# Optimization experiments

Measured on AMD Instinct MI355X. Metric: run time of the kernel, lower is better.

Reference implementation:

```python
import jax, jax.numpy as jnp
import numpy as np

D = 1024
H = 16
DH = D // H


def setup_inputs() -> dict:
    key = jax.random.key(0)
    ks = jax.random.split(key, 7)
    s = 0.02
    return {
        "z": jax.random.normal(ks[0], (8, 1024, D), dtype=jnp.float32),
        "ln_w": jnp.ones((D,), dtype=jnp.float32),
        "ln_b": jnp.zeros((D,), dtype=jnp.float32),
        "W_qkv": jax.random.normal(ks[1], (D, 3 * D), dtype=jnp.float32) * s,
        "b_qkv": jnp.zeros((3 * D,), dtype=jnp.float32),
        "W_proj": jax.random.normal(ks[2], (D, D), dtype=jnp.float32) * s,
        "b_proj": jnp.zeros((D,), dtype=jnp.float32),
    }


def reference(z, ln_w, ln_b, W_qkv, b_qkv, W_proj, b_proj):
    b, n, d = z.shape
    # Pre-LN
    mu = jnp.mean(z, axis=-1, keepdims=True)
    var = jnp.var(z, axis=-1, keepdims=True)
    zn = (z - mu) / jnp.sqrt(var + 1e-5) * ln_w + ln_b
    # QKV projection: [b, n, 3, H, DH]
    qkv = (zn @ W_qkv + b_qkv).reshape(b, n, 3, H, DH)
    q = qkv[:, :, 0].transpose(0, 2, 1, 3)  # [b, H, n, DH]
    k = qkv[:, :, 1].transpose(0, 2, 1, 3)
    v = qkv[:, :, 2].transpose(0, 2, 1, 3)
    scale = 1.0 / jnp.sqrt(jnp.asarray(DH, dtype=z.dtype))
    scores = jnp.einsum("bhqd,bhkd->bhqk", q, k) * scale
    attn = jax.nn.softmax(scores, axis=-1)
    msa = jnp.einsum("bhqk,bhkd->bhqd", attn, v)  # [b, H, n, DH]
    msa_cat = msa.transpose(0, 2, 1, 3).reshape(b, n, d)
    out = msa_cat @ W_proj + b_proj
    return z + out
```

## Files before the change

### kernel.cpp

```cpp
#include <hip/hip_runtime.h>
#include <stdint.h>

typedef unsigned short u16;
typedef uint8_t u8;
typedef __bf16 bf16x8 __attribute__((ext_vector_type(8)));
typedef float f32x4 __attribute__((ext_vector_type(4)));
typedef int i32x8 __attribute__((ext_vector_type(8)));

#define D_MODEL 1024
#define NHEADS  16
#define DHEAD   64
#define BATCH   8
#define SEQ     1024
#define MTOT    (BATCH*SEQ)

#define GPTR(p) ((const __attribute__((address_space(1))) void*)(p))
#define LPTR(p) ((__attribute__((address_space(3))) void*)(p))

#if defined(__HIP_DEVICE_COMPILE__)
  #define MFMA_FP8_16x16x128(a, b, c) \
      __builtin_amdgcn_mfma_scale_f32_16x16x128_f8f6f4((a), (b), (c), 0, 0, 0, 127, 0, 127)
  #define CVT_PK_FP8(a, b, old, w) __builtin_amdgcn_cvt_pk_fp8_f32((a), (b), (old), (w))
#else
  #define MFMA_FP8_16x16x128(a, b, c) (c)
  #define CVT_PK_FP8(a, b, old, w) (0)
#endif

__device__ __forceinline__ u16 f2bf(float f) {
    union { float f; uint32_t u; } v; v.f = f;
    uint32_t u = v.u;
    u += 0x7fffu + ((u >> 16) & 1u);
    return (u16)(u >> 16);
}

__device__ __forceinline__ uint32_t pklo(int i1, int i0) {
    return __builtin_amdgcn_perm((uint32_t)i1, (uint32_t)i0, 0x05040100u);
}

__global__ __launch_bounds__(256) void prep_inputs(
    const float* __restrict__ z, const float* __restrict__ w,
    const float* __restrict__ b, uint32_t* __restrict__ znf,
    const float* __restrict__ Wqkv, const float* __restrict__ Wproj,
    u8* __restrict__ outQkv, u8* __restrict__ outProj)
{
    __shared__ float red[8];
    __shared__ u8 tile[32][36];
    const int bid = blockIdx.x;
    const int t = threadIdx.x;
    if (bid < MTOT) {
        const int row = bid;
        const float4 v = reinterpret_cast<const float4*>(z + (size_t)row * D_MODEL)[t];
        float s  = v.x + v.y + v.z + v.w;
        float s2 = v.x*v.x + v.y*v.y + v.z*v.z + v.w*v.w;
        #pragma unroll
        for (int off = 32; off; off >>= 1) {
            s  += __shfl_down(s,  off, 64);
            s2 += __shfl_down(s2, off, 64);
        }
        const int wave = t >> 6, lane = t & 63;
        if (lane == 0) { red[wave] = s; red[wave + 4] = s2; }
        __syncthreads();
        if (t == 0) {
            float ts  = red[0] + red[1] + red[2] + red[3];
            float ts2 = red[4] + red[5] + red[6] + red[7];
            float mu  = ts * (1.0f / D_MODEL);
            float var = ts2 * (1.0f / D_MODEL) - mu * mu;
            red[0] = mu; red[1] = rsqrtf(var + 1e-5f);
        }
        __syncthreads();
        const float mu = red[0], rstd = red[1];
        const float4 wv = reinterpret_cast<const float4*>(w)[t];
        const float4 bv = reinterpret_cast<const float4*>(b)[t];
        const float x0 = (v.x - mu) * rstd * wv.x + bv.x;
        const float x1 = (v.y - mu) * rstd * wv.y + bv.y;
        const float x2 = (v.z - mu) * rstd * wv.z + bv.z;
        const float x3 = (v.w - mu) * rstd * wv.w + bv.w;
        int pk = CVT_PK_FP8(x0, x1, 0, false);
        pk = CVT_PK_FP8(x2, x3, pk, true);
        znf[(size_t)row * (D_MODEL / 4) + t] = (uint32_t)pk;
    } else {
        const int bx = bid - MTOT;
        const int cx = bx & 127;
        const int r0 = (bx >> 7) * 32;
        const float* in; u8* out; int C;
        if (cx < 96) { in = Wqkv;  out = outQkv;  C = 3072; }
        else         { in = Wproj; out = outProj; C = 1024; }
        const int c0 = (cx < 96 ? cx : cx - 96) * 32;
        const int tx = t & 31, ty = t >> 5;
        #pragma unroll
        for (int i = 0; i < 4; ++i) {
            const float f = in[(size_t)(r0 + ty + i*8) * C + c0 + tx];
            tile[ty + i*8][tx] = (u8)(CVT_PK_FP8(f, 0.f, 0, false) & 0xFF);
        }
        __syncthreads();
        #pragma unroll
        for (int i = 0; i < 4; ++i)
            out[(size_t)(c0 + ty + i*8) * D_MODEL + r0 + tx] = tile[tx][ty + i*8];
    }
}

#define QSCALE 23.0831207f

#define GEMM_PRELUDE                                                            \
    const int tid = threadIdx.x;                                                \
    const int wave = tid >> 6, lane = tid & 63;                                 \
    const int lm = lane & 15, g = lane >> 4;                                    \
    const int wm = (wave >> 1) * 64, wn = (wave & 1) * 64;                      \
    const int m0 = blockIdx.y * 128;                                            \
    const int srow = tid >> 3;                                                  \
    const int sseg = tid & 7;                                                   \
    const int sgcol = (sseg ^ (srow & 7)) * 16;                                 \
    const int xl = lm & 7;                                                      \
    const int ca0 = ((2 * g) ^ xl) * 16;                                        \
    const int ca1 = ((2 * g + 1) ^ xl) * 16;

#define FP8_KLOOP(As_, Bs_, A_, Bt_, n0_, MFMA_STMT)                            \
    f32x4 acc[4][4] = {};                                                       \
    for (int k0 = 0; k0 < D_MODEL; k0 += 128) {                                 \
        _Pragma("unroll")                                                       \
        for (int c = 0; c < 4; ++c) {                                           \
            const int r = srow + c * 32;                                        \
            __builtin_amdgcn_global_load_lds(                                   \
                GPTR(&A_[(size_t)(m0 + r) * D_MODEL + k0 + sgcol]),             \
                LPTR(&As_[r * 128 + sseg * 16]), 16, 0, 0);                     \
            __builtin_amdgcn_global_load_lds(                                   \
                GPTR(&Bt_[(size_t)((n0_) + r) * D_MODEL + k0 + sgcol]),         \
                LPTR(&Bs_[r * 128 + sseg * 16]), 16, 0, 0);                     \
        }                                                                       \
        __syncthreads();                                                        \
        i32x8 af[4], bfr[4];                                                    \
        _Pragma("unroll")                                                       \
        for (int i = 0; i < 4; ++i) {                                           \
            const uint4 alo = *reinterpret_cast<const uint4*>(&As_[(wm + i*16 + lm) * 128 + ca0]); \
            const uint4 ahi = *reinterpret_cast<const uint4*>(&As_[(wm + i*16 + lm) * 128 + ca1]); \
            af[i][0] = alo.x; af[i][1] = alo.y; af[i][2] = alo.z; af[i][3] = alo.w; \
            af[i][4] = ahi.x; af[i][5] = ahi.y; af[i][6] = ahi.z; af[i][7] = ahi.w; \
            const uint4 blo = *reinterpret_cast<const uint4*>(&Bs_[(wn + i*16 + lm) * 128 + ca0]); \
            const uint4 bhi = *reinterpret_cast<const uint4*>(&Bs_[(wn + i*16 + lm) * 128 + ca1]); \
            bfr[i][0] = blo.x; bfr[i][1] = blo.y; bfr[i][2] = blo.z; bfr[i][3] = blo.w; \
            bfr[i][4] = bhi.x; bfr[i][5] = bhi.y; bfr[i][6] = bhi.z; bfr[i][7] = bhi.w; \
        }                                                                       \
        _Pragma("unroll")                                                       \
        for (int i = 0; i < 4; ++i)                                             \
            _Pragma("unroll")                                                   \
            for (int j = 0; j < 4; ++j)                                         \
                MFMA_STMT;                                                      \
        __syncthreads();                                                        \
    }

__global__ __launch_bounds__(256, 2) void gemm_qkv(
    const u8* __restrict__ A, const u8* __restrict__ Bt,
    const float* __restrict__ bias,
    u16* __restrict__ q, u16* __restrict__ k, u16* __restrict__ vT)
{
    __shared__ u8 As[128 * 128];
    __shared__ u8 Bs[128 * 128];
    GEMM_PRELUDE
    const int bx = blockIdx.x;
    if (bx < 16) {
        const int n0 = bx * 128;
        FP8_KLOOP(As, Bs, A, Bt, n0, acc[i][j] = MFMA_FP8_16x16x128(bfr[j], af[i], acc[i][j]))
        const int colbase = n0 + wn;
        const int sel = colbase >> 10;
        const int h = (colbase & 1023) >> 6;
        u16* dst = (sel == 0) ? q : k;
        const float scl = (sel == 0) ? QSCALE : 1.0f;
        #pragma unroll
        for (int j = 0; j < 4; ++j) {
            const int dh0 = j * 16 + 4 * g;
            const float4 bv4 = *reinterpret_cast<const float4*>(&bias[colbase + dh0]);
            #pragma unroll
            for (int i = 0; i < 4; ++i) {
                const int m = m0 + wm + i * 16 + lm;
                const int b = m >> 10, t = m & 1023;
                ushort4 o;
                o.x = f2bf((acc[i][j][0] + bv4.x) * scl);
                o.y = f2bf((acc[i][j][1] + bv4.y) * scl);
                o.z = f2bf((acc[i][j][2] + bv4.z) * scl);
                o.w = f2bf((acc[i][j][3] + bv4.w) * scl);
                *reinterpret_cast<ushort4*>(
                    &dst[(((size_t)(b * NHEADS + h)) * SEQ + t) * DHEAD + dh0]) = o;
            }
        }
    } else {
        const int n0 = 2048 + (bx - 16) * 128;
        FP8_KLOOP(As, Bs, A, Bt, n0, acc[i][j] = MFMA_FP8_16x16x128(af[i], bfr[j], acc[i][j]))
        const int vcol = (n0 - 2048) + wn;
        const int h = vcol >> 6;
        #pragma unroll
        for (int j = 0; j < 4; ++j) {
            const int dh = ((vcol & 63) + j * 16) + lm;
            const float bv = bias[2048 + vcol + j * 16 + lm];
            #pragma unroll
            for (int i = 0; i < 4; ++i) {
                const int t0 = m0 + wm + i * 16 + 4 * g;
                const int b = t0 >> 10, t = t0 & 1023;
                ushort4 o;
                o.x = f2bf(acc[i][j][0] + bv);
                o.y = f2bf(acc[i][j][1] + bv);
                o.z = f2bf(acc[i][j][2] + bv);
                o.w = f2bf(acc[i][j][3] + bv);
                *reinterpret_cast<ushort4*>(
                    &vT[(((size_t)(b * NHEADS + h)) * DHEAD + dh) * SEQ + t]) = o;
            }
        }
    }
}

__global__ __launch_bounds__(256, 2) void gemm_proj(
    const u8* __restrict__ A, const u8* __restrict__ Bt,
    const float* __restrict__ bias, const float* __restrict__ z,
    float* __restrict__ out)
{
    __shared__ u8 As[128 * 128];
    __shared__ u8 Bs[128 * 128];
    GEMM_PRELUDE
    const int n0 = blockIdx.x * 128;
    FP8_KLOOP(As, Bs, A, Bt, n0, acc[i][j] = MFMA_FP8_16x16x128(bfr[j], af[i], acc[i][j]))
    #pragma unroll
    for (int j = 0; j < 4; ++j) {
        const int col0 = n0 + wn + j * 16 + 4 * g;
        const float4 bv4 = *reinterpret_cast<const float4*>(&bias[col0]);
        #pragma unroll
        for (int i = 0; i < 4; ++i) {
            const int m = m0 + wm + i * 16 + lm;
            const size_t idx = (size_t)m * D_MODEL + col0;
            const float4 zv = *reinterpret_cast<const float4*>(&z[idx]);
            float4 ov;
            ov.x = zv.x + acc[i][j][0] + bv4.x;
            ov.y = zv.y + acc[i][j][1] + bv4.y;
            ov.z = zv.z + acc[i][j][2] + bv4.z;
            ov.w = zv.w + acc[i][j][3] + bv4.w;
            *reinterpret_cast<float4*>(&out[idx]) = ov;
        }
    }
}

#define KLD 68
#define EXP2_MAGIC 12582912.0f

__global__ __launch_bounds__(256, 4) void attn_kernel(
    const u16* __restrict__ Q, const u16* __restrict__ K,
    const u16* __restrict__ Vt, u8* __restrict__ msaf)
{
    __shared__ u16 Ks[2][64 * KLD];
    __shared__ u16 Vs[2][64 * KLD];
    const int tid = threadIdx.x, wave = tid >> 6, lane = tid & 63;
    const int lm = lane & 15, g = lane >> 4;
    const int bi = blockIdx.x;
    const int bh = bi & 127;
    const int q0 = (bi >> 7) * 128;
    const int b = bh >> 4, h = bh & 15;
    const size_t headBase = (size_t)bh * SEQ * DHEAD;
    const u16* Qh = Q + headBase;
    const u16* Kh = K + headBase;
    const u16* Vh = Vt + headBase;

    const int srow = tid >> 3, sseg = tid & 7;
    const int aA = 16 * (sseg >> 2) + 4 * (sseg & 3);

    const uint4 onesu = {0x3F803F80u, 0x3F803F80u, 0x3F803F80u, 0x3F803F80u};
    const bf16x8 ONES = __builtin_bit_cast(bf16x8, onesu);
    const f32x4 SMINIT = {16250.0f, 16250.0f, 16250.0f, 16250.0f};

    bf16x8 qf[2][2];
    #pragma unroll
    for (int s = 0; s < 2; ++s) {
        const u16* qrow = Qh + (size_t)(q0 + s * 64 + wave * 16 + lm) * DHEAD;
        qf[s][0] = *reinterpret_cast<const bf16x8*>(qrow + g * 8);
        qf[s][1] = *reinterpret_cast<const bf16x8*>(qrow + 32 + g * 8);
    }

    f32x4 o[2][4] = {};
    f32x4 lacc[2] = {};

    for (int j0 = 0; j0 < SEQ; j0 += 128) {
        #pragma unroll
        for (int hb = 0; hb < 2; ++hb) {
            const int jj = j0 + hb * 64;
            #pragma unroll
            for (int s2 = 0; s2 < 2; ++s2) {
                const int row = srow + 32 * s2;
                *reinterpret_cast<uint4*>(&Ks[hb][row * KLD + sseg * 8]) =
                    *reinterpret_cast<const uint4*>(&Kh[(size_t)(jj + row) * DHEAD + sseg * 8]);
                const u16* vrow = Vh + (size_t)row * SEQ + jj;
                const uint2 va = *reinterpret_cast<const uint2*>(vrow + aA);
                const uint2 vb = *reinterpret_cast<const uint2*>(vrow + 32 + aA);
                uint4 wv; wv.x = va.x; wv.y = va.y; wv.z = vb.x; wv.w = vb.y;
                *reinterpret_cast<uint4*>(&Vs[hb][row * KLD + sseg * 8]) = wv;
            }
        }
        __syncthreads();

        #pragma unroll
        for (int hb = 0; hb < 2; ++hb) {
            bf16x8 kf0[4], kf1[4];
            #pragma unroll
            for (int ni = 0; ni < 4; ++ni) {
                kf0[ni] = *reinterpret_cast<const bf16x8*>(&Ks[hb][(ni*16 + lm) * KLD + g * 8]);
                kf1[ni] = *reinterpret_cast<const bf16x8*>(&Ks[hb][(ni*16 + lm) * KLD + 32 + g * 8]);
            }

            bf16x8 pfr[2][2];
            #pragma unroll
            for (int s = 0; s < 2; ++s) {
                f32x4 st[4];
                __builtin_amdgcn_s_setprio(1);
                #pragma unroll
                for (int ni = 0; ni < 4; ++ni) {
                    st[ni] = __builtin_amdgcn_mfma_f32_16x16x32_bf16(kf0[ni], qf[s][0], SMINIT, 0, 0, 0);
                    st[ni] = __builtin_amdgcn_mfma_f32_16x16x32_bf16(kf1[ni], qf[s][1], st[ni], 0, 0, 0);
                }
                __builtin_amdgcn_s_setprio(0);
                int ip[4][4];
                #pragma unroll
                for (int ni = 0; ni < 4; ++ni)
                    #pragma unroll
                    for (int r = 0; r < 4; ++r)
                        ip[ni][r] = __builtin_bit_cast(int, st[ni][r] + EXP2_MAGIC);
                #pragma unroll
                for (int c = 0; c < 2; ++c) {
                    uint4 u;
                    u.x = pklo(ip[c][1],   ip[c][0]);
                    u.y = pklo(ip[c][3],   ip[c][2]);
                    u.z = pklo(ip[c+2][1], ip[c+2][0]);
                    u.w = pklo(ip[c+2][3], ip[c+2][2]);
                    pfr[s][c] = __builtin_bit_cast(bf16x8, u);
                }
                lacc[s] = __builtin_amdgcn_mfma_f32_16x16x32_bf16(ONES, pfr[s][0], lacc[s], 0, 0, 0);
                lacc[s] = __builtin_amdgcn_mfma_f32_16x16x32_bf16(ONES, pfr[s][1], lacc[s], 0, 0, 0);
            }

            __builtin_amdgcn_s_setprio(1);
            #pragma unroll
            for (int mt = 0; mt < 4; ++mt) {
                bf16x8 vf0 = *reinterpret_cast<const bf16x8*>(&Vs[hb][(mt*16 + lm) * KLD + g * 8]);
                bf16x8 vf1 = *reinterpret_cast<const bf16x8*>(&Vs[hb][(mt*16 + lm) * KLD + 32 + g * 8]);
                #pragma unroll
                for (int s = 0; s < 2; ++s) {
                    o[s][mt] = __builtin_amdgcn_mfma_f32_16x16x32_bf16(vf0, pfr[s][0], o[s][mt], 0, 0, 0);
                    o[s][mt] = __builtin_amdgcn_mfma_f32_16x16x32_bf16(vf1, pfr[s][1], o[s][mt], 0, 0, 0);
                }
            }
            __builtin_amdgcn_s_setprio(0);
        }
        __syncthreads();
    }

    #pragma unroll
    for (int s = 0; s < 2; ++s) {
        const float inv = 1.0f / lacc[s][0];
        const int t = q0 + s * 64 + wave * 16 + lm;
        const size_t base = ((size_t)b * SEQ + t) * D_MODEL + h * DHEAD;
        #pragma unroll
        for (int mt = 0; mt < 4; ++mt) {
            const int d0 = mt * 16 + 4 * g;
            int pk = CVT_PK_FP8(o[s][mt][0] * inv, o[s][mt][1] * inv, 0, false);
            pk = CVT_PK_FP8(o[s][mt][2] * inv, o[s][mt][3] * inv, pk, true);
            *reinterpret_cast<uint32_t*>(&msaf[base + d0]) = (uint32_t)pk;
        }
    }
}

extern "C" void kernel_launch(void* const* d_in, const int* in_sizes, int n_in,
                              void* d_out, int out_size, void* d_ws, size_t ws_size,
                              hipStream_t stream) {
    const float* z      = (const float*)d_in[0];
    const float* ln_w   = (const float*)d_in[1];
    const float* ln_b   = (const float*)d_in[2];
    const float* W_qkv  = (const float*)d_in[3];
    const float* b_qkv  = (const float*)d_in[4];
    const float* W_proj = (const float*)d_in[5];
    const float* b_proj = (const float*)d_in[6];
    float* out = (float*)d_out;

    u8* ws = (u8*)d_ws;
    u8*  znf     = ws;
    u8*  wqkvTf  = znf + (size_t)MTOT * D_MODEL;
    u8*  wprojTf = wqkvTf + (size_t)3 * D_MODEL * D_MODEL;
    u8*  msaf    = wprojTf + (size_t)D_MODEL * D_MODEL;
    u16* q       = (u16*)(msaf + (size_t)MTOT * D_MODEL);
    u16* k       = q + (size_t)MTOT * D_MODEL;
    u16* vT      = k + (size_t)MTOT * D_MODEL;

    prep_inputs<<<MTOT + 4096, 256, 0, stream>>>(
        z, ln_w, ln_b, (uint32_t*)znf, W_qkv, W_proj, wqkvTf, wprojTf);
    gemm_qkv<<<dim3(24, MTOT / 128), 256, 0, stream>>>(znf, wqkvTf, b_qkv, q, k, vT);
    attn_kernel<<<BATCH * NHEADS * (SEQ / 128), 256, 0, stream>>>(q, k, vT, msaf);
    gemm_proj<<<dim3(D_MODEL / 128, MTOT / 128), 256, 0, stream>>>(
        msaf, wprojTf, b_proj, z, out);
}
```

Baseline: 206.3 us.

## Swizzle GEMM block order across XCDs and shrink attention KV tile to 64

Both GEMM kernels now remap the linear block index so that consecutive blocks landing on the same XCD (lin&7) cover neighbouring M/N tiles, aiming for better L2 reuse of A and B tiles. The attention kernel processes 64 keys per iteration instead of 128, halving LDS usage per block. Smaller LDS may allow more resident blocks, at the cost of twice as many barriers and loop iterations. The swizzle assumes the grid dimensions match the hardcoded 24x64 and 8x64 shapes.

Result: faster. 200.8 us (median of 2 runs) (-2.6%).

```diff
diff --git a/kernel.cpp b/kernel.cpp
--- a/kernel.cpp
+++ b/kernel.cpp
@@ -106,7 +106,6 @@
     const int wave = tid >> 6, lane = tid & 63;                                 \
     const int lm = lane & 15, g = lane >> 4;                                    \
     const int wm = (wave >> 1) * 64, wn = (wave & 1) * 64;                      \
-    const int m0 = blockIdx.y * 128;                                            \
     const int srow = tid >> 3;                                                  \
     const int sseg = tid & 7;                                                   \
     const int sgcol = (sseg ^ (srow & 7)) * 16;                                 \
@@ -156,7 +155,10 @@
     __shared__ u8 As[128 * 128];
     __shared__ u8 Bs[128 * 128];
     GEMM_PRELUDE
-    const int bx = blockIdx.x;
+    const int lin = blockIdx.y * 24 + blockIdx.x;
+    const int nl  = (lin & 7) * 192 + (lin >> 3);
+    const int bx  = nl % 24;
+    const int m0  = (nl / 24) * 128;
     if (bx < 16) {
         const int n0 = bx * 128;
         FP8_KLOOP(As, Bs, A, Bt, n0, acc[i][j] = MFMA_FP8_16x16x128(bfr[j], af[i], acc[i][j]))
@@ -215,7 +217,10 @@
     __shared__ u8 As[128 * 128];
     __shared__ u8 Bs[128 * 128];
     GEMM_PRELUDE
-    const int n0 = blockIdx.x * 128;
+    const int lin = blockIdx.y * 8 + blockIdx.x;
+    const int nl  = (lin & 7) * 64 + (lin >> 3);
+    const int n0  = (nl & 7) * 128;
+    const int m0  = (nl >> 3) * 128;
     FP8_KLOOP(As, Bs, A, Bt, n0, acc[i][j] = MFMA_FP8_16x16x128(bfr[j], af[i], acc[i][j]))
     #pragma unroll
     for (int j = 0; j < 4; ++j) {
@@ -243,8 +248,8 @@
     const u16* __restrict__ Q, const u16* __restrict__ K,
     const u16* __restrict__ Vt, u8* __restrict__ msaf)
 {
-    __shared__ u16 Ks[2][64 * KLD];
-    __shared__ u16 Vs[2][64 * KLD];
+    __shared__ u16 Ks[64 * KLD];
+    __shared__ u16 Vs[64 * KLD];
     const int tid = threadIdx.x, wave = tid >> 6, lane = tid & 63;
     const int lm = lane & 15, g = lane >> 4;
     const int bi = blockIdx.x;
@@ -274,76 +279,69 @@
     f32x4 o[2][4] = {};
     f32x4 lacc[2] = {};
 
-    for (int j0 = 0; j0 < SEQ; j0 += 128) {
-        #pragma unroll
-        for (int hb = 0; hb < 2; ++hb) {
-            const int jj = j0 + hb * 64;
-            #pragma unroll
-            for (int s2 = 0; s2 < 2; ++s2) {
-                const int row = srow + 32 * s2;
-                *reinterpret_cast<uint4*>(&Ks[hb][row * KLD + sseg * 8]) =
-                    *reinterpret_cast<const uint4*>(&Kh[(size_t)(jj + row) * DHEAD + sseg * 8]);
-                const u16* vrow = Vh + (size_t)row * SEQ + jj;
-                const uint2 va = *reinterpret_cast<const uint2*>(vrow + aA);
-                const uint2 vb = *reinterpret_cast<const uint2*>(vrow + 32 + aA);
-                uint4 wv; wv.x = va.x; wv.y = va.y; wv.z = vb.x; wv.w = vb.y;
-                *reinterpret_cast<uint4*>(&Vs[hb][row * KLD + sseg * 8]) = wv;
-            }
-        }
-        __syncthreads();
-
-        #pragma unroll
-        for (int hb = 0; hb < 2; ++hb) {
-            bf16x8 kf0[4], kf1[4];
+    for (int j0 = 0; j0 < SEQ; j0 += 64) {
+        #pragma unroll
+        for (int s2 = 0; s2 < 2; ++s2) {
+            const int row = srow + 32 * s2;
+            *reinterpret_cast<uint4*>(&Ks[row * KLD + sseg * 8]) =
+                *reinterpret_cast<const uint4*>(&Kh[(size_t)(j0 + row) * DHEAD + sseg * 8]);
+            const u16* vrow = Vh + (size_t)row * SEQ + j0;
+            const uint2 va = *reinterpret_cast<const uint2*>(vrow + aA);
+            const uint2 vb = *reinterpret_cast<const uint2*>(vrow + 32 + aA);
+            uint4 wv; wv.x = va.x; wv.y = va.y; wv.z = vb.x; wv.w = vb.y;
+            *reinterpret_cast<uint4*>(&Vs[row * KLD + sseg * 8]) = wv;
+        }
+        __syncthreads();
+
+        bf16x8 kf0[4], kf1[4];
+        #pragma unroll
+        for (int ni = 0; ni < 4; ++ni) {
+            kf0[ni] = *reinterpret_cast<const bf16x8*>(&Ks[(ni*16 + lm) * KLD + g * 8]);
+            kf1[ni] = *reinterpret_cast<const bf16x8*>(&Ks[(ni*16 + lm) * KLD + 32 + g * 8]);
+        }
+
+        bf16x8 pfr[2][2];
+        #pragma unroll
+        for (int s = 0; s < 2; ++s) {
+            f32x4 st[4];
+            __builtin_amdgcn_s_setprio(1);
             #pragma unroll
             for (int ni = 0; ni < 4; ++ni) {
-                kf0[ni] = *reinterpret_cast<const bf16x8*>(&Ks[hb][(ni*16 + lm) * KLD + g * 8]);
-                kf1[ni] = *reinterpret_cast<const bf16x8*>(&Ks[hb][(ni*16 + lm) * KLD + 32 + g * 8]);
-            }
-
-            bf16x8 pfr[2][2];
+                st[ni] = __builtin_amdgcn_mfma_f32_16x16x32_bf16(kf0[ni], qf[s][0], SMINIT, 0, 0, 0);
+                st[ni] = __builtin_amdgcn_mfma_f32_16x16x32_bf16(kf1[ni], qf[s][1], st[ni], 0, 0, 0);
+            }
+            __builtin_amdgcn_s_setprio(0);
+            int ip[4][4];
+            #pragma unroll
+            for (int ni = 0; ni < 4; ++ni)
+                #pragma unroll
+                for (int r = 0; r < 4; ++r)
+                    ip[ni][r] = __builtin_bit_cast(int, st[ni][r] + EXP2_MAGIC);
+            #pragma unroll
+            for (int c = 0; c < 2; ++c) {
+                uint4 u;
+                u.x = pklo(ip[c][1],   ip[c][0]);
+                u.y = pklo(ip[c][3],   ip[c][2]);
+                u.z = pklo(ip[c+2][1], ip[c+2][0]);
+                u.w = pklo(ip[c+2][3], ip[c+2][2]);
+                pfr[s][c] = __builtin_bit_cast(bf16x8, u);
+            }
+            lacc[s] = __builtin_amdgcn_mfma_f32_16x16x32_bf16(ONES, pfr[s][0], lacc[s], 0, 0, 0);
+            lacc[s] = __builtin_amdgcn_mfma_f32_16x16x32_bf16(ONES, pfr[s][1], lacc[s], 0, 0, 0);
+        }
+
+        __builtin_amdgcn_s_setprio(1);
+        #pragma unroll
+        for (int mt = 0; mt < 4; ++mt) {
+            bf16x8 vf0 = *reinterpret_cast<const bf16x8*>(&Vs[(mt*16 + lm) * KLD + g * 8]);
+            bf16x8 vf1 = *reinterpret_cast<const bf16x8*>(&Vs[(mt*16 + lm) * KLD + 32 + g * 8]);
             #pragma unroll
             for (int s = 0; s < 2; ++s) {
-                f32x4 st[4];
-                __builtin_amdgcn_s_setprio(1);
-                #pragma unroll
-                for (int ni = 0; ni < 4; ++ni) {
-                    st[ni] = __builtin_amdgcn_mfma_f32_16x16x32_bf16(kf0[ni], qf[s][0], SMINIT, 0, 0, 0);
-                    st[ni] = __builtin_amdgcn_mfma_f32_16x16x32_bf16(kf1[ni], qf[s][1], st[ni], 0, 0, 0);
-                }
-                __builtin_amdgcn_s_setprio(0);
-                int ip[4][4];
-                #pragma unroll
-                for (int ni = 0; ni < 4; ++ni)
-                    #pragma unroll
-                    for (int r = 0; r < 4; ++r)
-                        ip[ni][r] = __builtin_bit_cast(int, st[ni][r] + EXP2_MAGIC);
-                #pragma unroll
-                for (int c = 0; c < 2; ++c) {
-                    uint4 u;
-                    u.x = pklo(ip[c][1],   ip[c][0]);
-                    u.y = pklo(ip[c][3],   ip[c][2]);
-                    u.z = pklo(ip[c+2][1], ip[c+2][0]);
-                    u.w = pklo(ip[c+2][3], ip[c+2][2]);
-                    pfr[s][c] = __builtin_bit_cast(bf16x8, u);
-                }
-                lacc[s] = __builtin_amdgcn_mfma_f32_16x16x32_bf16(ONES, pfr[s][0], lacc[s], 0, 0, 0);
-                lacc[s] = __builtin_amdgcn_mfma_f32_16x16x32_bf16(ONES, pfr[s][1], lacc[s], 0, 0, 0);
-            }
-
-            __builtin_amdgcn_s_setprio(1);
-            #pragma unroll
-            for (int mt = 0; mt < 4; ++mt) {
-                bf16x8 vf0 = *reinterpret_cast<const bf16x8*>(&Vs[hb][(mt*16 + lm) * KLD + g * 8]);
-                bf16x8 vf1 = *reinterpret_cast<const bf16x8*>(&Vs[hb][(mt*16 + lm) * KLD + 32 + g * 8]);
-                #pragma unroll
-                for (int s = 0; s < 2; ++s) {
-                    o[s][mt] = __builtin_amdgcn_mfma_f32_16x16x32_bf16(vf0, pfr[s][0], o[s][mt], 0, 0, 0);
-                    o[s][mt] = __builtin_amdgcn_mfma_f32_16x16x32_bf16(vf1, pfr[s][1], o[s][mt], 0, 0, 0);
-                }
-            }
-            __builtin_amdgcn_s_setprio(0);
-        }
+                o[s][mt] = __builtin_amdgcn_mfma_f32_16x16x32_bf16(vf0, pfr[s][0], o[s][mt], 0, 0, 0);
+                o[s][mt] = __builtin_amdgcn_mfma_f32_16x16x32_bf16(vf1, pfr[s][1], o[s][mt], 0, 0, 0);
+            }
+        }
+        __builtin_amdgcn_s_setprio(0);
         __syncthreads();
     }
 
```
